# Performance work log

Measured on AMD Instinct MI355X. Metric: run time of the kernel, lower is better.

Reference implementation:

```python
import jax, jax.numpy as jnp
import numpy as np

NUM_AA = 21  # amino-acid alphabet size


def setup_inputs() -> dict:
    key = jax.random.key(0)
    k_x, k_q, k_k, k_v = jax.random.split(key, 4)
    B, L, H, D = 64, 512, 32, 128
    x = jax.random.randint(k_x, (B, L), 0, NUM_AA, dtype=jnp.int32)
    Q = jax.random.normal(k_q, (H, L, D), dtype=jnp.float32)
    K = jax.random.normal(k_k, (H, L, D), dtype=jnp.float32)
    V = jax.random.normal(k_v, (H, NUM_AA, NUM_AA), dtype=jnp.float32)
    return {"x": x, "Q": Q, "K": K, "V": V}


def reference(x, Q, K, V):
    # x: [B, L] int indices in [0, 21); Q,K: [H, L, d_k]; V: [H, q, q]
    d_k = Q.shape[-1]
    L = Q.shape[1]
    # attention over positions, per head: [H, L, L]
    scores = jnp.einsum('hid,hjd->hij', Q, K) / d_k
    A = jax.nn.softmax(scores, axis=-1)
    # coupling tensor J[i, j, a, b] = sum_h A[h, i, j] * V[h, a, b]  -> [L, L, q, q]
    J = jnp.einsum('hij,hab->ijab', A, V)
    # energy[b] = -sum_{i,j} J[i, j, x[b,i], x[b,j]]
    ii = jnp.arange(L)[:, None]        # [L, 1]
    jj = jnp.arange(L)[None, :]        # [1, L]
    vals = J[ii, jj, x[:, :, None], x[:, None, :]]  # broadcast gather -> [B, L, L]
    energy = -jnp.sum(vals, axis=(1, 2))            # [B]
    return energy
```

## Files before the change

kernel.cpp:

```cpp
#include <hip/hip_runtime.h>
#include <hip/hip_bf16.h>
#include <stdint.h>

#define NH  32
#define NL  512
#define ND  128
#define NB  64
#define NAA 21

#define EW_OFF 0
#define QB_OFF (16u << 20)
#define KB_OFF (18u << 20)
#define ZG_OFF (20u << 20)
#define BF_OFF (21u << 20)

typedef short bf16x8 __attribute__((ext_vector_type(8)));
typedef float f32x4  __attribute__((ext_vector_type(4)));

static __device__ __forceinline__ uint32_t bf16rtn(float f) {
    uint32_t u = __float_as_uint(f);
    return (u + 0x7fffu + ((u >> 16) & 1u)) >> 16;
}
static __device__ __forceinline__ void gl16(const void* g, void* l) {
    __builtin_amdgcn_global_load_lds(
        (const __attribute__((address_space(1))) uint32_t*)g,
        (__attribute__((address_space(3))) uint32_t*)l, 16, 0, 0);
}

__global__ void prep_qk(const float* __restrict__ Q, const float* __restrict__ K,
                        uint32_t* __restrict__ Qb, uint32_t* __restrict__ Kb) {
    uint32_t tid = blockIdx.x * 256 + threadIdx.x;
    const float* src = (tid >> 20) ? K : Q;
    uint32_t*    dst = (tid >> 20) ? Kb : Qb;
    uint32_t p = tid & 0xFFFFFu;
    uint32_t kk2 = p & 31, r = (p >> 5) & 63, dc = (p >> 11) & 1;
    uint32_t pt = (p >> 12) & 7, h = p >> 15;
    uint32_t pos = pt * 64 + r, d0 = dc * 64 + kk2 * 2;
    float2 v = *(const float2*)(src + ((size_t)(h * NL + pos) * ND + d0));
    uint32_t val = bf16rtn(v.x) | (bf16rtn(v.y) << 16);
    uint32_t byte = (r * 128 + kk2 * 4) ^ ((r & 7) << 4);
    dst[((((h * 8 + pt) * 2 + dc)) << 11) + (byte >> 2)] = val;
}

__global__ void prep_bfrag(const int* __restrict__ x, uint8_t* __restrict__ Bf) {
    int tid = blockIdx.x * 256 + threadIdx.x;
    int lane = tid & 63;
    int f  = tid >> 6;
    int cg = f % 12;
    int t2 = f / 12;
    int ks = t2 & 1;
    int t3 = t2 >> 1;
    int kc = t3 & 7;
    int nb = t3 >> 3;
    int col = nb * 192 + cg * 16 + (lane & 15);
    int b = col / 21, c = col - b * 21;
    int k0 = kc * 64 + ks * 32 + (lane >> 4) * 8;
    const int* xp = x + (size_t)b * NL + k0;
    int4 x0 = *(const int4*)(xp);
    int4 x1 = *(const int4*)(xp + 4);
    uint4 pk;
    pk.x = ((x0.x == c) ? 0x3F80u : 0u) | ((x0.y == c) ? 0x3F800000u : 0u);
    pk.y = ((x0.z == c) ? 0x3F80u : 0u) | ((x0.w == c) ? 0x3F800000u : 0u);
    pk.z = ((x1.x == c) ? 0x3F80u : 0u) | ((x1.y == c) ? 0x3F800000u : 0u);
    pk.w = ((x1.z == c) ? 0x3F80u : 0u) | ((x1.w == c) ? 0x3F800000u : 0u);
    *(uint4*)(Bf + (size_t)tid * 16) = pk;
}

#define SC_QS 0
#define SC_KS 16384
#define SC_ZS 49152
#define SC_TOT 49408

__global__ __launch_bounds__(512)
void scores_mfma(const uint8_t* __restrict__ Qb, const uint8_t* __restrict__ Kb,
                 uint8_t* __restrict__ Ewsw, float* __restrict__ Zg) {
    extern __shared__ uint8_t smem[];
    int h = blockIdx.x >> 3, it = blockIdx.x & 7;
    int t = threadIdx.x, lane = t & 63, wv = t >> 6;
    int wm = wv >> 1, wn = wv & 1;

    const uint8_t* qsrc = Qb + (((size_t)(h * 8 + it) * 2) << 13);
    gl16(qsrc + t * 16,        smem + SC_QS + t * 16);
    gl16(qsrc + 8192 + t * 16, smem + SC_QS + 8192 + t * 16);
    if (t < 64) *(float*)(smem + SC_ZS + t * 4) = 0.f;

    float zp[2] = {0.f, 0.f};
    for (int sc = 0; sc < 4; ++sc) {
        __syncthreads();
        const uint8_t* ksrc = Kb + (((size_t)(h * 8 + sc * 2) * 2) << 13);
#pragma unroll
        for (int q = 0; q < 4; ++q)
            gl16(ksrc + q * 8192 + t * 16, smem + SC_KS + q * 8192 + t * 16);
        __syncthreads();

        f32x4 acc[2][2];
#pragma unroll
        for (int fm = 0; fm < 2; ++fm)
#pragma unroll
            for (int fn = 0; fn < 2; ++fn) acc[fm][fn] = (f32x4){0.f,0.f,0.f,0.f};

#pragma unroll
        for (int ks = 0; ks < 4; ++ks) {
            int kb = ((ks & 1) * 32 + (lane >> 4) * 8) * 2;
            int dc = ks >> 1;
            bf16x8 af[2], bfr[2];
#pragma unroll
            for (int fm = 0; fm < 2; ++fm) {
                int rr = wm * 32 + fm * 16 + (lane & 15);
                int rt = rr >> 6, r6 = rr & 63;
                af[fm] = *(bf16x8*)(smem + SC_KS + (rt * 2 + dc) * 8192 +
                          (((uint32_t)(r6 * 128 + kb)) ^ ((r6 & 7) << 4)));
            }
#pragma unroll
            for (int fn = 0; fn < 2; ++fn) {
                int rr = wn * 32 + fn * 16 + (lane & 15);
                bfr[fn] = *(bf16x8*)(smem + SC_QS + dc * 8192 +
                          (((uint32_t)(rr * 128 + kb)) ^ ((rr & 7) << 4)));
            }
#pragma unroll
            for (int fm = 0; fm < 2; ++fm)
#pragma unroll
                for (int fn = 0; fn < 2; ++fn)
                    acc[fm][fn] = __builtin_amdgcn_mfma_f32_16x16x32_bf16(
                        af[fm], bfr[fn], acc[fm][fn], 0, 0, 0);
        }
#pragma unroll
        for (int fm = 0; fm < 2; ++fm)
#pragma unroll
            for (int fn = 0; fn < 2; ++fn) {
                float e0 = __expf(acc[fm][fn][0] * 0.0078125f);
                float e1 = __expf(acc[fm][fn][1] * 0.0078125f);
                float e2 = __expf(acc[fm][fn][2] * 0.0078125f);
                float e3 = __expf(acc[fm][fn][3] * 0.0078125f);
                zp[fn] += (e0 + e1) + (e2 + e3);
                uint2 pk;
                pk.x = bf16rtn(e0) | (bf16rtn(e1) << 16);
                pk.y = bf16rtn(e2) | (bf16rtn(e3) << 16);
                int j = sc * 128 + wm * 32 + fm * 16 + (lane >> 4) * 4;
                int i = wn * 32 + fn * 16 + (lane & 15);
                int kc = j >> 6, kk = j & 63;
                uint32_t byte = ((uint32_t)(i * 128 + kk * 2)) ^ ((uint32_t)((i & 7) << 4));
                *(uint2*)(Ewsw + (((size_t)((h * 8 + it) * 8 + kc)) << 13) + byte) = pk;
            }
    }
    zp[0] += __shfl_xor(zp[0], 16); zp[0] += __shfl_xor(zp[0], 32);
    zp[1] += __shfl_xor(zp[1], 16); zp[1] += __shfl_xor(zp[1], 32);
    if (lane < 16) {
        atomicAdd((float*)(smem + SC_ZS) + wn * 32 + lane,      zp[0]);
        atomicAdd((float*)(smem + SC_ZS) + wn * 32 + 16 + lane, zp[1]);
    }
    __syncthreads();
    if (t < 64) Zg[(size_t)h * NL + it * 64 + t] = *((float*)(smem + SC_ZS) + t);
}

#define GE_AB   0
#define GE_RACC 0
#define GE_XS   32768
#define GE_VS   38016
#define GE_TOT  39808

__global__ __launch_bounds__(512, 4)
void gemm_energy(const uint8_t* __restrict__ Ew, const uint8_t* __restrict__ Bf,
                 const int* __restrict__ x, const float* __restrict__ Zg,
                 const float* __restrict__ V, float* __restrict__ out) {
    extern __shared__ uint8_t smem[];
    uint32_t* xs = (uint32_t*)(smem + GE_XS);
    float*    Vs = (float*)(smem + GE_VS);
    float*    Racc = (float*)(smem + GE_RACC);

    int bid = blockIdx.x;
    int xcd = bid & 7, q = bid >> 3;
    int nb = q % 7, g = (q / 7) * 8 + xcd;
    int h = g >> 2, it = g & 3;
    int n0 = nb * 192;
    int bstart = n0 / 21;
    int bend = (n0 + 191) / 21;
    int bcnt = bend - bstart + 1;

    int t = threadIdx.x, lane = t & 63, wv = t >> 6;
    int wm = wv >> 2, wn = wv & 3;

    const uint8_t* A0 = Ew + (((size_t)(h * 8 + it * 2) * 8) << 13);
    const uint8_t* A1 = Ew + (((size_t)(h * 8 + it * 2 + 1) * 8) << 13);
#define GE_STAGE(p, kc) do { \
        gl16(A0 + (((size_t)(kc)) << 13) + t * 16, smem + GE_AB + (p) * 16384 + t * 16); \
        gl16(A1 + (((size_t)(kc)) << 13) + t * 16, smem + GE_AB + (p) * 16384 + 8192 + t * 16); \
    } while (0)
    GE_STAGE(0, 0);

    for (int idx = t; idx < bcnt * 128; idx += 512) {
        int s = idx >> 7, w = idx & 127;
        int4 xv = *(const int4*)(x + (size_t)(bstart + s) * NL + w * 4);
        xs[s * 129 + w] = (uint32_t)(xv.x & 0xff) | ((uint32_t)(xv.y & 0xff) << 8)
                        | ((uint32_t)(xv.z & 0xff) << 16) | ((uint32_t)(xv.w & 0xff) << 24);
    }
    for (int idx = t; idx < NAA * NAA; idx += 512) Vs[idx] = V[h * (NAA * NAA) + idx];

    const uint8_t* bfw = Bf + ((size_t)(nb * 192 + 3 * wn)) * 1024 + lane * 16;

    uint32_t aoff[2][4];
#pragma unroll
    for (int ks = 0; ks < 2; ++ks)
#pragma unroll
        for (int fm = 0; fm < 4; ++fm) {
            int r6 = fm * 16 + (lane & 15);
            int kb = (ks * 32 + (lane >> 4) * 8) * 2;
            aoff[ks][fm] = (uint32_t)(wm * 8192 +
                           (((uint32_t)(r6 * 128 + kb)) ^ ((r6 & 7) << 4)));
        }

    f32x4 acc[4][3];
#pragma unroll
    for (int fm = 0; fm < 4; ++fm)
#pragma unroll
        for (int fn = 0; fn < 3; ++fn) acc[fm][fn] = (f32x4){0.f,0.f,0.f,0.f};

    __syncthreads();

    for (int kc = 0; kc < 8; ++kc) {
        int p = kc & 1;
        if (kc < 7) GE_STAGE(p ^ 1, kc + 1);
        bf16x8 bfr[2][3];
#pragma unroll
        for (int ks = 0; ks < 2; ++ks)
#pragma unroll
            for (int fn = 0; fn < 3; ++fn)
                bfr[ks][fn] = *(const bf16x8*)(bfw + kc * 24576 + ks * 12288 + fn * 1024);
#pragma unroll
        for (int ks = 0; ks < 2; ++ks) {
            bf16x8 af[4];
#pragma unroll
            for (int fm = 0; fm < 4; ++fm)
                af[fm] = *(bf16x8*)(smem + GE_AB + p * 16384 + aoff[ks][fm]);
#pragma unroll
            for (int fm = 0; fm < 4; ++fm)
#pragma unroll
                for (int fn = 0; fn < 3; ++fn)
                    acc[fm][fn] = __builtin_amdgcn_mfma_f32_16x16x32_bf16(
                        af[fm], bfr[ks][fn], acc[fm][fn], 0, 0, 0);
        }
        __syncthreads();
    }

    float vsum = 0.f;
    int srow = lane & 31;
    int s = wv * 2 + (lane >> 5);
#pragma unroll
    for (int w = 0; w < 4; ++w) {
        if (wm == (w >> 1)) {
#pragma unroll
            for (int f = 0; f < 2; ++f) {
                int fm = (w & 1) * 2 + f;
#pragma unroll
                for (int fn = 0; fn < 3; ++fn) {
                    int col = wn * 48 + fn * 16 + (lane & 15);
                    int rb = f * 16 + (lane >> 4) * 4;
#pragma unroll
                    for (int r = 0; r < 4; ++r)
                        Racc[(rb + r) * 193 + col] = acc[fm][fn][r];
                }
            }
        }
        __syncthreads();
        int ig = it * 128 + w * 32 + srow;
        float rz = 1.0f / Zg[(size_t)h * NL + ig];
        if (s < bcnt) {
            int b = bstart + s;
            uint32_t xw = xs[s * 129 + (ig >> 2)];
            int a = (int)((xw >> ((ig & 3) * 8)) & 0xffu);
            int off = b * 21 - n0;
            int clo = off < 0 ? -off : 0;
            int chi = (192 - off) < 21 ? (192 - off) : 21;
            float dot = 0.f;
            for (int c = clo; c < chi; ++c)
                dot += Vs[a * NAA + c] * Racc[srow * 193 + off + c];
            vsum += dot * rz;
        }
        __syncthreads();
    }
#pragma unroll
    for (int o = 1; o < 32; o <<= 1) vsum += __shfl_xor(vsum, o);
    if (srow == 0 && s < bcnt) atomicAdd(&out[bstart + s], -vsum);
}

extern "C" void kernel_launch(void* const* d_in, const int* in_sizes, int n_in,
                              void* d_out, int out_size, void* d_ws, size_t ws_size,
                              hipStream_t stream) {
    const int*   x = (const int*)d_in[0];
    const float* Q = (const float*)d_in[1];
    const float* K = (const float*)d_in[2];
    const float* V = (const float*)d_in[3];
    float* out = (float*)d_out;
    uint8_t* ws = (uint8_t*)d_ws;

    uint8_t*  Ewsw = ws + EW_OFF;
    uint32_t* Qb   = (uint32_t*)(ws + QB_OFF);
    uint32_t* Kb   = (uint32_t*)(ws + KB_OFF);
    float*    Zg   = (float*)(ws + ZG_OFF);
    uint8_t*  Bfr  = ws + BF_OFF;

    hipMemsetAsync(d_out, 0, NB * sizeof(float), stream);
    prep_qk<<<8192, 256, 0, stream>>>(Q, K, Qb, Kb);
    prep_bfrag<<<336, 256, 0, stream>>>(x, Bfr);
    (void)hipFuncSetAttribute((const void*)scores_mfma,
                              hipFuncAttributeMaxDynamicSharedMemorySize, SC_TOT);
    scores_mfma<<<256, 512, SC_TOT, stream>>>((const uint8_t*)Qb, (const uint8_t*)Kb,
                                              Ewsw, Zg);
    (void)hipFuncSetAttribute((const void*)gemm_energy,
                              hipFuncAttributeMaxDynamicSharedMemorySize, GE_TOT);
    gemm_energy<<<896, 512, GE_TOT, stream>>>((const uint8_t*)Ewsw, Bfr, x, Zg, V, out);
}
```

Before: 78.73 us.

## Load A operand directly from global memory instead of staging through LDS

Result: slower. 89.15 us (+13.2%).

```diff
diff --git a/kernel.cpp b/kernel.cpp
--- a/kernel.cpp
+++ b/kernel.cpp
@@ -153,13 +153,12 @@
     if (t < 64) Zg[(size_t)h * NL + it * 64 + t] = *((float*)(smem + SC_ZS) + t);
 }
 
-#define GE_AB   0
 #define GE_RACC 0
-#define GE_XS   32768
-#define GE_VS   38016
-#define GE_TOT  39808
-
-__global__ __launch_bounds__(512, 4)
+#define GE_XS   24704
+#define GE_VS   29952
+#define GE_TOT  31744
+
+__global__ __launch_bounds__(512)
 void gemm_energy(const uint8_t* __restrict__ Ew, const uint8_t* __restrict__ Bf,
                  const int* __restrict__ x, const float* __restrict__ Zg,
                  const float* __restrict__ V, float* __restrict__ out) {
@@ -180,14 +179,6 @@
     int t = threadIdx.x, lane = t & 63, wv = t >> 6;
     int wm = wv >> 2, wn = wv & 3;
 
-    const uint8_t* A0 = Ew + (((size_t)(h * 8 + it * 2) * 8) << 13);
-    const uint8_t* A1 = Ew + (((size_t)(h * 8 + it * 2 + 1) * 8) << 13);
-#define GE_STAGE(p, kc) do { \
-        gl16(A0 + (((size_t)(kc)) << 13) + t * 16, smem + GE_AB + (p) * 16384 + t * 16); \
-        gl16(A1 + (((size_t)(kc)) << 13) + t * 16, smem + GE_AB + (p) * 16384 + 8192 + t * 16); \
-    } while (0)
-    GE_STAGE(0, 0);
-
     for (int idx = t; idx < bcnt * 128; idx += 512) {
         int s = idx >> 7, w = idx & 127;
         int4 xv = *(const int4*)(x + (size_t)(bstart + s) * NL + w * 4);
@@ -196,18 +187,17 @@
     }
     for (int idx = t; idx < NAA * NAA; idx += 512) Vs[idx] = V[h * (NAA * NAA) + idx];
 
-    const uint8_t* bfw = Bf + ((size_t)(nb * 192 + 3 * wn)) * 1024 + lane * 16;
-
-    uint32_t aoff[2][4];
+    const uint8_t* Aw = Ew + (((size_t)((h * 8 + it * 2 + wm) * 8)) << 13);
+    uint32_t aswz[2][4];
 #pragma unroll
     for (int ks = 0; ks < 2; ++ks)
 #pragma unroll
         for (int fm = 0; fm < 4; ++fm) {
             int r6 = fm * 16 + (lane & 15);
             int kb = (ks * 32 + (lane >> 4) * 8) * 2;
-            aoff[ks][fm] = (uint32_t)(wm * 8192 +
-                           (((uint32_t)(r6 * 128 + kb)) ^ ((r6 & 7) << 4)));
+            aswz[ks][fm] = ((uint32_t)(r6 * 128 + kb)) ^ ((uint32_t)((r6 & 7) << 4));
         }
+    const uint8_t* bfw = Bf + ((size_t)(nb * 192 + 3 * wn)) * 1024 + lane * 16;
 
     f32x4 acc[4][3];
 #pragma unroll
@@ -217,30 +207,29 @@
 
     __syncthreads();
 
+#pragma unroll
     for (int kc = 0; kc < 8; ++kc) {
-        int p = kc & 1;
-        if (kc < 7) GE_STAGE(p ^ 1, kc + 1);
-        bf16x8 bfr[2][3];
+        bf16x8 af[2][4], bfr[2][3];
+#pragma unroll
+        for (int ks = 0; ks < 2; ++ks)
+#pragma unroll
+            for (int fm = 0; fm < 4; ++fm)
+                af[ks][fm] = *(const bf16x8*)(Aw + ((uint32_t)kc << 13) + aswz[ks][fm]);
 #pragma unroll
         for (int ks = 0; ks < 2; ++ks)
 #pragma unroll
             for (int fn = 0; fn < 3; ++fn)
                 bfr[ks][fn] = *(const bf16x8*)(bfw + kc * 24576 + ks * 12288 + fn * 1024);
 #pragma unroll
-        for (int ks = 0; ks < 2; ++ks) {
-            bf16x8 af[4];
-#pragma unroll
-            for (int fm = 0; fm < 4; ++fm)
-                af[fm] = *(bf16x8*)(smem + GE_AB + p * 16384 + aoff[ks][fm]);
+        for (int ks = 0; ks < 2; ++ks)
 #pragma unroll
             for (int fm = 0; fm < 4; ++fm)
 #pragma unroll
                 for (int fn = 0; fn < 3; ++fn)
                     acc[fm][fn] = __builtin_amdgcn_mfma_f32_16x16x32_bf16(
-                        af[fm], bfr[ks][fn], acc[fm][fn], 0, 0, 0);
-        }
-        __syncthreads();
-    }
+                        af[ks][fm], bfr[ks][fn], acc[fm][fn], 0, 0, 0);
+    }
+    __syncthreads();
 
     float vsum = 0.f;
     int srow = lane & 31;
```

## Halve gemm_energy block to 4 waves, each computing all 128 rows

Applied to the files above, without the earlier changes.

Result: slower. 82.25 us (+4.5%).

```diff
diff --git a/kernel.cpp b/kernel.cpp
--- a/kernel.cpp
+++ b/kernel.cpp
@@ -159,7 +159,7 @@
 #define GE_VS   38016
 #define GE_TOT  39808
 
-__global__ __launch_bounds__(512, 4)
+__global__ __launch_bounds__(256, 3)
 void gemm_energy(const uint8_t* __restrict__ Ew, const uint8_t* __restrict__ Bf,
                  const int* __restrict__ x, const float* __restrict__ Zg,
                  const float* __restrict__ V, float* __restrict__ out) {
@@ -178,40 +178,31 @@
     int bcnt = bend - bstart + 1;
 
     int t = threadIdx.x, lane = t & 63, wv = t >> 6;
-    int wm = wv >> 2, wn = wv & 3;
+    int wn = wv;
 
     const uint8_t* A0 = Ew + (((size_t)(h * 8 + it * 2) * 8) << 13);
     const uint8_t* A1 = Ew + (((size_t)(h * 8 + it * 2 + 1) * 8) << 13);
 #define GE_STAGE(p, kc) do { \
-        gl16(A0 + (((size_t)(kc)) << 13) + t * 16, smem + GE_AB + (p) * 16384 + t * 16); \
-        gl16(A1 + (((size_t)(kc)) << 13) + t * 16, smem + GE_AB + (p) * 16384 + 8192 + t * 16); \
+        gl16(A0 + (((size_t)(kc)) << 13) + t * 16,        smem + GE_AB + (p) * 16384 + t * 16); \
+        gl16(A0 + (((size_t)(kc)) << 13) + 4096 + t * 16, smem + GE_AB + (p) * 16384 + 4096 + t * 16); \
+        gl16(A1 + (((size_t)(kc)) << 13) + t * 16,        smem + GE_AB + (p) * 16384 + 8192 + t * 16); \
+        gl16(A1 + (((size_t)(kc)) << 13) + 4096 + t * 16, smem + GE_AB + (p) * 16384 + 12288 + t * 16); \
     } while (0)
     GE_STAGE(0, 0);
 
-    for (int idx = t; idx < bcnt * 128; idx += 512) {
+    for (int idx = t; idx < bcnt * 128; idx += 256) {
         int s = idx >> 7, w = idx & 127;
         int4 xv = *(const int4*)(x + (size_t)(bstart + s) * NL + w * 4);
         xs[s * 129 + w] = (uint32_t)(xv.x & 0xff) | ((uint32_t)(xv.y & 0xff) << 8)
                         | ((uint32_t)(xv.z & 0xff) << 16) | ((uint32_t)(xv.w & 0xff) << 24);
     }
-    for (int idx = t; idx < NAA * NAA; idx += 512) Vs[idx] = V[h * (NAA * NAA) + idx];
+    for (int idx = t; idx < NAA * NAA; idx += 256) Vs[idx] = V[h * (NAA * NAA) + idx];
 
     const uint8_t* bfw = Bf + ((size_t)(nb * 192 + 3 * wn)) * 1024 + lane * 16;
 
-    uint32_t aoff[2][4];
-#pragma unroll
-    for (int ks = 0; ks < 2; ++ks)
-#pragma unroll
-        for (int fm = 0; fm < 4; ++fm) {
-            int r6 = fm * 16 + (lane & 15);
-            int kb = (ks * 32 + (lane >> 4) * 8) * 2;
-            aoff[ks][fm] = (uint32_t)(wm * 8192 +
-                           (((uint32_t)(r6 * 128 + kb)) ^ ((r6 & 7) << 4)));
-        }
-
-    f32x4 acc[4][3];
-#pragma unroll
-    for (int fm = 0; fm < 4; ++fm)
+    f32x4 acc[8][3];
+#pragma unroll
+    for (int fm = 0; fm < 8; ++fm)
 #pragma unroll
         for (int fn = 0; fn < 3; ++fn) acc[fm][fn] = (f32x4){0.f,0.f,0.f,0.f};
 
@@ -228,41 +219,44 @@
                 bfr[ks][fn] = *(const bf16x8*)(bfw + kc * 24576 + ks * 12288 + fn * 1024);
 #pragma unroll
         for (int ks = 0; ks < 2; ++ks) {
-            bf16x8 af[4];
-#pragma unroll
-            for (int fm = 0; fm < 4; ++fm)
-                af[fm] = *(bf16x8*)(smem + GE_AB + p * 16384 + aoff[ks][fm]);
-#pragma unroll
-            for (int fm = 0; fm < 4; ++fm)
-#pragma unroll
-                for (int fn = 0; fn < 3; ++fn)
-                    acc[fm][fn] = __builtin_amdgcn_mfma_f32_16x16x32_bf16(
-                        af[fm], bfr[ks][fn], acc[fm][fn], 0, 0, 0);
-        }
-        __syncthreads();
-    }
-
-    float vsum = 0.f;
-    int srow = lane & 31;
-    int s = wv * 2 + (lane >> 5);
-#pragma unroll
-    for (int w = 0; w < 4; ++w) {
-        if (wm == (w >> 1)) {
-#pragma unroll
-            for (int f = 0; f < 2; ++f) {
-                int fm = (w & 1) * 2 + f;
-#pragma unroll
-                for (int fn = 0; fn < 3; ++fn) {
-                    int col = wn * 48 + fn * 16 + (lane & 15);
-                    int rb = f * 16 + (lane >> 4) * 4;
-#pragma unroll
-                    for (int r = 0; r < 4; ++r)
-                        Racc[(rb + r) * 193 + col] = acc[fm][fn][r];
+            int kb = (ks * 32 + (lane >> 4) * 8) * 2;
+#pragma unroll
+            for (int half = 0; half < 2; ++half) {
+                bf16x8 af[4];
+#pragma unroll
+                for (int fq = 0; fq < 4; ++fq) {
+                    int fm = half * 4 + fq;
+                    int rr = fm * 16 + (lane & 15);
+                    int rt = rr >> 6, r6 = rr & 63;
+                    af[fq] = *(bf16x8*)(smem + GE_AB + p * 16384 + rt * 8192 +
+                              (((uint32_t)(r6 * 128 + kb)) ^ ((r6 & 7) << 4)));
                 }
+#pragma unroll
+                for (int fq = 0; fq < 4; ++fq)
+#pragma unroll
+                    for (int fn = 0; fn < 3; ++fn)
+                        acc[half * 4 + fq][fn] = __builtin_amdgcn_mfma_f32_16x16x32_bf16(
+                            af[fq], bfr[ks][fn], acc[half * 4 + fq][fn], 0, 0, 0);
             }
         }
         __syncthreads();
-        int ig = it * 128 + w * 32 + srow;
+    }
+
+    float vsum = 0.f;
+    int srow = lane & 15;
+    int s = wv * 4 + (lane >> 4);
+#pragma unroll
+    for (int w = 0; w < 8; ++w) {
+#pragma unroll
+        for (int fn = 0; fn < 3; ++fn) {
+            int col = wn * 48 + fn * 16 + (lane & 15);
+            int rb = (lane >> 4) * 4;
+#pragma unroll
+            for (int r = 0; r < 4; ++r)
+                Racc[(rb + r) * 193 + col] = acc[w][fn][r];
+        }
+        __syncthreads();
+        int ig = it * 128 + w * 16 + srow;
         float rz = 1.0f / Zg[(size_t)h * NL + ig];
         if (s < bcnt) {
             int b = bstart + s;
@@ -279,7 +273,7 @@
         __syncthreads();
     }
 #pragma unroll
-    for (int o = 1; o < 32; o <<= 1) vsum += __shfl_xor(vsum, o);
+    for (int o = 1; o < 16; o <<= 1) vsum += __shfl_xor(vsum, o);
     if (srow == 0 && s < bcnt) atomicAdd(&out[bstart + s], -vsum);
 }
 
@@ -308,5 +302,5 @@
                                               Ewsw, Zg);
     (void)hipFuncSetAttribute((const void*)gemm_energy,
                               hipFuncAttributeMaxDynamicSharedMemorySize, GE_TOT);
-    gemm_energy<<<896, 512, GE_TOT, stream>>>((const uint8_t*)Ewsw, Bfr, x, Zg, V, out);
-}
+    gemm_energy<<<896, 256, GE_TOT, stream>>>((const uint8_t*)Ewsw, Bfr, x, Zg, V, out);
+}
```
